# Performance work log

Measured on AMD Instinct MI355X. Metric: run time of the kernel, lower is better.

The kernel has to match this reference:

```python
import jax, jax.numpy as jnp
import numpy as np

HM = 256  # output_hm_shape


def _peak_grid(heatmap):
    # max_num_peaks=1 NMS -> global argmax per (b, joint) channel
    B, J, H, W = heatmap.shape
    idx = jnp.argmax(heatmap.reshape(B, J, H * W), axis=-1)
    y = (idx // W).astype(jnp.float32)
    x = (idx % W).astype(jnp.float32)
    ny = (H - 1) / 2.0
    nx = (W - 1) / 2.0
    # normalized (gx, gy) in [-1, 1], note (row,col) -> (x,y) flip as in source
    return jnp.stack([(x - nx) / nx, (y - ny) / ny], axis=-1)  # [B, J, 2]


def _bilinear_sample(feat, grid):
    # feat: [B, C, H, W], grid: [B, N, 2] (gx, gy), align_corners=True
    B, C, H, W = feat.shape
    x = (grid[..., 0] + 1.0) * 0.5 * (W - 1)
    y = (grid[..., 1] + 1.0) * 0.5 * (H - 1)
    x0 = jnp.floor(x); y0 = jnp.floor(y)
    wx = x - x0; wy = y - y0
    x0i = jnp.clip(x0, 0, W - 1).astype(jnp.int32)
    x1i = jnp.clip(x0 + 1, 0, W - 1).astype(jnp.int32)
    y0i = jnp.clip(y0, 0, H - 1).astype(jnp.int32)
    y1i = jnp.clip(y0 + 1, 0, H - 1).astype(jnp.int32)
    ff = feat.reshape(B, C, H * W)
    def g(iy, ix):
        return jnp.take_along_axis(ff, (iy * W + ix)[:, None, :], axis=2)  # [B, C, N]
    wx = wx[:, None, :]; wy = wy[:, None, :]
    return (g(y0i, x0i) * (1 - wx) * (1 - wy) + g(y0i, x1i) * wx * (1 - wy)
            + g(y1i, x0i) * (1 - wx) * wy + g(y1i, x1i) * wx * wy)


def _nearest_sample(feat, grid):
    B, C, H, W = feat.shape
    ix = jnp.clip(jnp.round((grid[..., 0] + 1.0) * 0.5 * (W - 1)), 0, W - 1).astype(jnp.int32)
    iy = jnp.clip(jnp.round((grid[..., 1] + 1.0) * 0.5 * (H - 1)), 0, H - 1).astype(jnp.int32)
    ff = feat.reshape(B, C, H * W)
    return jnp.take_along_axis(ff, (iy * W + ix)[:, None, :], axis=2)  # [B, C, N]


def _mlp(x, Ws, bs):
    # ReLU on every layer including last (is_activation_last=True)
    for W, b in zip(Ws, bs):
        x = jax.nn.relu(x @ W + b)
    return x


def setup_inputs() -> dict:
    key = jax.random.key(0)
    ks = jax.random.split(key, 16)
    inp = {
        'heatmap': jax.random.normal(ks[0], (16, 64, HM, HM), jnp.float32),
        'pos_embed': jax.random.normal(ks[1], (16, 32, HM, HM), jnp.float32),
        'feat1': jax.random.normal(ks[2], (16, 96, 128, 128), jnp.float32),
        'feat2': jax.random.normal(ks[3], (16, 384, 64, 64), jnp.float32),
        'feat3': jax.random.normal(ks[4], (16, 512, 32, 32), jnp.float32),
    }
    dims = [992, 1024, 512, 256, 224]
    for i in range(4):
        fan = dims[i]
        inp[f'W{i+1}'] = jax.random.normal(ks[5 + i], (dims[i], dims[i + 1]), jnp.float32) / np.sqrt(fan)
        inp[f'b{i+1}'] = jnp.zeros((dims[i + 1],), jnp.float32)
    return inp


def reference(heatmap, pos_embed, feat1, feat2, feat3, W1, b1, W2, b2, W3, b3, W4, b4):
    grid = _peak_grid(heatmap)  # [B, J, 2], detached in original (cpu numpy)
    positions = _nearest_sample(pos_embed, grid)  # [B, 32, J]
    ms = jnp.concatenate([_bilinear_sample(feat1, grid),
                          _bilinear_sample(feat2, grid),
                          _bilinear_sample(feat3, grid)], axis=1)  # [B, 992, J]
    seq = _mlp(ms.transpose(0, 2, 1), [W1, W2, W3, W4], [b1, b2, b3, b4])  # [B, J, 224]
    input_seq = jnp.concatenate([seq.transpose(0, 2, 1), positions], axis=1)  # [B, 256, J]
    return input_seq
```

## Files before the change

kernel.cpp:

```cpp
#include <hip/hip_runtime.h>
#include <hip/hip_bf16.h>
#include <cstddef>
#include <cstdint>


typedef __attribute__((ext_vector_type(8))) short bf16x8;
typedef __attribute__((ext_vector_type(4))) float f32x4;

__device__ inline void bilinear_block(const float* __restrict__ fb, int C, int H, int W,
                                      float gx, float gy,
                                      __hip_bfloat16* __restrict__ dst, int tid) {
    const float x = (gx + 1.0f) * 0.5f * (float)(W - 1);
    const float y = (gy + 1.0f) * 0.5f * (float)(H - 1);
    const float x0f = floorf(x), y0f = floorf(y);
    const float wx = x - x0f, wy = y - y0f;
    const int x0 = (int)fminf(fmaxf(x0f,       0.f), (float)(W - 1));
    const int x1 = (int)fminf(fmaxf(x0f + 1.f, 0.f), (float)(W - 1));
    const int y0 = (int)fminf(fmaxf(y0f,       0.f), (float)(H - 1));
    const int y1 = (int)fminf(fmaxf(y0f + 1.f, 0.f), (float)(H - 1));
    const float w00 = (1.f - wx) * (1.f - wy);
    const float w01 = wx * (1.f - wy);
    const float w10 = (1.f - wx) * wy;
    const float w11 = wx * wy;
    const int i00 = y0 * W + x0, i01 = y0 * W + x1;
    const int i10 = y1 * W + x0, i11 = y1 * W + x1;
    const size_t HW = (size_t)H * W;
    for (int c = tid; c < C; c += 256) {
        const float* fc = fb + (size_t)c * HW;
        float v = fc[i00] * w00 + fc[i01] * w01 + fc[i10] * w10 + fc[i11] * w11;
        dst[c] = __float2bfloat16(v);
    }
}

__global__ __launch_bounds__(256) void fused_front_kernel(
    const float* __restrict__ hm,
    const float* __restrict__ pos_embed,
    const float* __restrict__ feat1, const float* __restrict__ feat2,
    const float* __restrict__ feat3,
    const float* __restrict__ W1, const float* __restrict__ W2,
    const float* __restrict__ W3, const float* __restrict__ W4,
    __hip_bfloat16* __restrict__ T1, __hip_bfloat16* __restrict__ T2,
    __hip_bfloat16* __restrict__ T3, __hip_bfloat16* __restrict__ T4,
    __hip_bfloat16* __restrict__ X0, float* __restrict__ out) {
    __shared__ float smem[32 * 33];
    float* sval = smem;
    int*   sidx = (int*)(smem + 4);
    const int tid = threadIdx.x;

    if (blockIdx.x >= 1024) {
        int bid = blockIdx.x - 1024;
        const float* W; __hip_bfloat16* T; int K, N;
        if (bid < 992)        { W = W1; T = T1; K = 992;  N = 1024; }
        else if (bid < 1504)  { bid -= 992;  W = W2; T = T2; K = 1024; N = 512; }
        else if (bid < 1632)  { bid -= 1504; W = W3; T = T3; K = 512;  N = 256; }
        else                  { bid -= 1632; W = W4; T = T4; K = 256;  N = 224; }
        const int tilesN = N >> 5;
        const int tk = bid / tilesN, tn = bid - tk * tilesN;
        float (*tile)[33] = (float(*)[33])smem;
        const int col = tid & 31, rowg = tid >> 5;
        #pragma unroll
        for (int i = 0; i < 4; ++i) {
            int k = (tk << 5) + rowg + (i << 3);
            tile[rowg + (i << 3)][col] = W[(size_t)k * N + (tn << 5) + col];
        }
        __syncthreads();
        #pragma unroll
        for (int i = 0; i < 4; ++i) {
            int n = (tn << 5) + rowg + (i << 3);
            T[(size_t)n * K + (tk << 5) + col] = __float2bfloat16(tile[col][rowg + (i << 3)]);
        }
        return;
    }

    const int plane = blockIdx.x;
    const float4* p4 = (const float4*)(hm + (size_t)plane * 65536);
    float best = -3.402823466e38f;
    int bidx = 0;
    for (int i = tid; i < 16384; i += 256) {
        float4 v = p4[i];
        int base = i << 2;
        if (v.x > best) { best = v.x; bidx = base; }
        if (v.y > best) { best = v.y; bidx = base + 1; }
        if (v.z > best) { best = v.z; bidx = base + 2; }
        if (v.w > best) { best = v.w; bidx = base + 3; }
    }
    #pragma unroll
    for (int off = 32; off > 0; off >>= 1) {
        float ov = __shfl_down(best, off);
        int   oi = __shfl_down(bidx, off);
        if (ov > best || (ov == best && oi < bidx)) { best = ov; bidx = oi; }
    }
    if ((tid & 63) == 0) { sval[tid >> 6] = best; sidx[tid >> 6] = bidx; }
    __syncthreads();
    float bv = sval[0]; int bi = sidx[0];
    #pragma unroll
    for (int w2 = 1; w2 < 4; ++w2) {
        float ov = sval[w2]; int oi = sidx[w2];
        if (ov > bv || (ov == bv && oi < bi)) { bv = ov; bi = oi; }
    }
    const int idx = bi;

    const int b = plane >> 6, j = plane & 63;
    const int py = idx >> 8, px = idx & 255;
    const float gx = ((float)px - 127.5f) / 127.5f;
    const float gy = ((float)py - 127.5f) / 127.5f;

    if (tid < 32) {
        float v = pos_embed[((size_t)(b * 32 + tid)) * 65536 + idx];
        out[(size_t)b * 16384 + (size_t)(224 + tid) * 64 + j] = v;
    }

    __hip_bfloat16* xrow = X0 + (size_t)plane * 992;
    bilinear_block(feat1 + (size_t)b *  96 * 128 * 128,  96, 128, 128, gx, gy, xrow,       tid);
    bilinear_block(feat2 + (size_t)b * 384 *  64 *  64, 384,  64,  64, gx, gy, xrow +  96, tid);
    bilinear_block(feat3 + (size_t)b * 512 *  32 *  32, 512,  32,  32, gx, gy, xrow + 480, tid);
}

template<bool LAST>
__global__ __launch_bounds__(256) void mfma_gemm_sk(
    const short* __restrict__ A, const short* __restrict__ Bt,
    const float* __restrict__ bias, void* __restrict__ Yv,
    int N, int K) {
    __shared__ float red[4 * 64 * 17];
    const int tid = threadIdx.x;
    const int w = tid >> 6, lane = tid & 63;
    const int q = lane >> 4, r = lane & 15;
    const int m0 = blockIdx.y << 5;
    const int n0 = blockIdx.x << 5;

    const short* pa0 = A  + (size_t)(m0 + r) * K + (q << 3);
    const short* pa1 = pa0 + (size_t)16 * K;
    const short* pb0 = Bt + (size_t)(n0 + r) * K + (q << 3);
    const short* pb1 = pb0 + (size_t)16 * K;

    f32x4 acc00 = {0.f,0.f,0.f,0.f}, acc01 = {0.f,0.f,0.f,0.f};
    f32x4 acc10 = {0.f,0.f,0.f,0.f}, acc11 = {0.f,0.f,0.f,0.f};

    const int nk = K >> 5;
    int ks = w;
    {
        int off = ks << 5;
        bf16x8 a0 = *(const bf16x8*)(pa0 + off);
        bf16x8 a1 = *(const bf16x8*)(pa1 + off);
        bf16x8 b0 = *(const bf16x8*)(pb0 + off);
        bf16x8 b1 = *(const bf16x8*)(pb1 + off);
        for (ks += 4; ks < nk; ks += 4) {
            int o2 = ks << 5;
            bf16x8 na0 = *(const bf16x8*)(pa0 + o2);
            bf16x8 na1 = *(const bf16x8*)(pa1 + o2);
            bf16x8 nb0 = *(const bf16x8*)(pb0 + o2);
            bf16x8 nb1 = *(const bf16x8*)(pb1 + o2);
            acc00 = __builtin_amdgcn_mfma_f32_16x16x32_bf16(a0, b0, acc00, 0, 0, 0);
            acc01 = __builtin_amdgcn_mfma_f32_16x16x32_bf16(a0, b1, acc01, 0, 0, 0);
            acc10 = __builtin_amdgcn_mfma_f32_16x16x32_bf16(a1, b0, acc10, 0, 0, 0);
            acc11 = __builtin_amdgcn_mfma_f32_16x16x32_bf16(a1, b1, acc11, 0, 0, 0);
            a0 = na0; a1 = na1; b0 = nb0; b1 = nb1;
        }
        acc00 = __builtin_amdgcn_mfma_f32_16x16x32_bf16(a0, b0, acc00, 0, 0, 0);
        acc01 = __builtin_amdgcn_mfma_f32_16x16x32_bf16(a0, b1, acc01, 0, 0, 0);
        acc10 = __builtin_amdgcn_mfma_f32_16x16x32_bf16(a1, b0, acc10, 0, 0, 0);
        acc11 = __builtin_amdgcn_mfma_f32_16x16x32_bf16(a1, b1, acc11, 0, 0, 0);
    }

    float* myrow = red + (size_t)(w * 64 + lane) * 17;
    #pragma unroll
    for (int i = 0; i < 4; ++i) {
        myrow[i]      = acc00[i];
        myrow[4 + i]  = acc01[i];
        myrow[8 + i]  = acc10[i];
        myrow[12 + i] = acc11[i];
    }
    __syncthreads();

    #pragma unroll
    for (int jj = 0; jj < 4; ++jj) {
        const int e = tid + (jj << 8);
        const int le = e >> 4, s = e & 15;
        const int which = s >> 2, i = s & 3;
        float v = red[(0 * 64 + le) * 17 + s] + red[(1 * 64 + le) * 17 + s]
                + red[(2 * 64 + le) * 17 + s] + red[(3 * 64 + le) * 17 + s];
        const int qe = le >> 4, re = le & 15;
        const int row = m0 + (qe << 2) + i + ((which & 2) ? 16 : 0);
        const int col = n0 + re + ((which & 1) ? 16 : 0);
        v = fmaxf(v + bias[col], 0.f);
        if (LAST) {
            float* O = (float*)Yv;
            O[(size_t)(row >> 6) * 16384 + (size_t)col * 64 + (row & 63)] = v;
        } else {
            __hip_bfloat16* Y = (__hip_bfloat16*)Yv;
            Y[(size_t)row * N + col] = __float2bfloat16(v);
        }
    }
}

extern "C" void kernel_launch(void* const* d_in, const int* in_sizes, int n_in,
                              void* d_out, int out_size, void* d_ws, size_t ws_size,
                              hipStream_t stream) {
    (void)in_sizes; (void)n_in; (void)out_size; (void)ws_size;
    const float* heatmap   = (const float*)d_in[0];
    const float* pos_embed = (const float*)d_in[1];
    const float* feat1     = (const float*)d_in[2];
    const float* feat2     = (const float*)d_in[3];
    const float* feat3     = (const float*)d_in[4];
    const float* W1 = (const float*)d_in[5];  const float* b1 = (const float*)d_in[6];
    const float* W2 = (const float*)d_in[7];  const float* b2 = (const float*)d_in[8];
    const float* W3 = (const float*)d_in[9];  const float* b3 = (const float*)d_in[10];
    const float* W4 = (const float*)d_in[11]; const float* b4 = (const float*)d_in[12];
    float* out = (float*)d_out;

    char* ws = (char*)d_ws;
    short* X0 = (short*)(ws + 8192);
    short* X1 = X0 + (size_t)1024 * 992;
    short* X2 = X1 + (size_t)1024 * 1024;
    short* X3 = X2 + (size_t)1024 * 512;
    short* T1 = X3 + (size_t)1024 * 256;
    short* T2 = T1 + (size_t)1024 * 992;
    short* T3 = T2 + (size_t)512 * 1024;
    short* T4 = T3 + (size_t)256 * 512;

    fused_front_kernel<<<2712, 256, 0, stream>>>(
        heatmap, pos_embed, feat1, feat2, feat3,
        W1, W2, W3, W4,
        (__hip_bfloat16*)T1, (__hip_bfloat16*)T2, (__hip_bfloat16*)T3, (__hip_bfloat16*)T4,
        (__hip_bfloat16*)X0, out);
    mfma_gemm_sk<false><<<dim3(32, 32), 256, 0, stream>>>(X0, T1, b1, X1, 1024,  992);
    mfma_gemm_sk<false><<<dim3(16, 32), 256, 0, stream>>>(X1, T2, b2, X2,  512, 1024);
    mfma_gemm_sk<false><<<dim3( 8, 32), 256, 0, stream>>>(X2, T3, b3, X3,  256,  512);
    mfma_gemm_sk<true ><<<dim3( 7, 32), 256, 0, stream>>>(X3, T4, b4, out,  224,  256);
}
```

Measured before the change: 578.1 us.

## Merge front and four GEMM launches into one cooperative persistent kernel

Replaces the front kernel and the four GEMM kernel launches with a single cooperative kernel of 512 blocks. The blocks loop over argmax planes, weight transposes and GEMM tiles, with grid.sync between layers. GEMM tiles are resized per layer so each stage has about 1024 tiles. This removes launch gaps and tail effects between kernels, but it halves the parallelism of the bandwidth-bound heatmap argmax phase and adds grid-wide barrier cost.

```diff
diff --git a/kernel.cpp b/kernel.cpp
--- a/kernel.cpp
+++ b/kernel.cpp
@@ -1,15 +1,18 @@
 #include <hip/hip_runtime.h>
+#include <hip/hip_cooperative_groups.h>
 #include <hip/hip_bf16.h>
 #include <cstddef>
 #include <cstdint>
 
+namespace cg = cooperative_groups;
+
 
 typedef __attribute__((ext_vector_type(8))) short bf16x8;
 typedef __attribute__((ext_vector_type(4))) float f32x4;
 
-__device__ inline void bilinear_block(const float* __restrict__ fb, int C, int H, int W,
-                                      float gx, float gy,
-                                      __hip_bfloat16* __restrict__ dst, int tid) {
+__device__ __forceinline__ void bilinear_block(const float* __restrict__ fb, int C, int H, int W,
+                                               float gx, float gy,
+                                               __hip_bfloat16* __restrict__ dst, int tid) {
     const float x = (gx + 1.0f) * 0.5f * (float)(W - 1);
     const float y = (gy + 1.0f) * 0.5f * (float)(H - 1);
     const float x0f = floorf(x), y0f = floorf(y);
@@ -32,156 +35,87 @@
     }
 }
 
-__global__ __launch_bounds__(256) void fused_front_kernel(
-    const float* __restrict__ hm,
-    const float* __restrict__ pos_embed,
-    const float* __restrict__ feat1, const float* __restrict__ feat2,
-    const float* __restrict__ feat3,
-    const float* __restrict__ W1, const float* __restrict__ W2,
-    const float* __restrict__ W3, const float* __restrict__ W4,
-    __hip_bfloat16* __restrict__ T1, __hip_bfloat16* __restrict__ T2,
-    __hip_bfloat16* __restrict__ T3, __hip_bfloat16* __restrict__ T4,
-    __hip_bfloat16* __restrict__ X0, float* __restrict__ out) {
-    __shared__ float smem[32 * 33];
-    float* sval = smem;
-    int*   sidx = (int*)(smem + 4);
-    const int tid = threadIdx.x;
-
-    if (blockIdx.x >= 1024) {
-        int bid = blockIdx.x - 1024;
-        const float* W; __hip_bfloat16* T; int K, N;
-        if (bid < 992)        { W = W1; T = T1; K = 992;  N = 1024; }
-        else if (bid < 1504)  { bid -= 992;  W = W2; T = T2; K = 1024; N = 512; }
-        else if (bid < 1632)  { bid -= 1504; W = W3; T = T3; K = 512;  N = 256; }
-        else                  { bid -= 1632; W = W4; T = T4; K = 256;  N = 224; }
-        const int tilesN = N >> 5;
-        const int tk = bid / tilesN, tn = bid - tk * tilesN;
-        float (*tile)[33] = (float(*)[33])smem;
-        const int col = tid & 31, rowg = tid >> 5;
-        #pragma unroll
-        for (int i = 0; i < 4; ++i) {
-            int k = (tk << 5) + rowg + (i << 3);
-            tile[rowg + (i << 3)][col] = W[(size_t)k * N + (tn << 5) + col];
-        }
-        __syncthreads();
-        #pragma unroll
-        for (int i = 0; i < 4; ++i) {
-            int n = (tn << 5) + rowg + (i << 3);
-            T[(size_t)n * K + (tk << 5) + col] = __float2bfloat16(tile[col][rowg + (i << 3)]);
-        }
-        return;
-    }
-
-    const int plane = blockIdx.x;
-    const float4* p4 = (const float4*)(hm + (size_t)plane * 65536);
-    float best = -3.402823466e38f;
-    int bidx = 0;
-    for (int i = tid; i < 16384; i += 256) {
-        float4 v = p4[i];
-        int base = i << 2;
-        if (v.x > best) { best = v.x; bidx = base; }
-        if (v.y > best) { best = v.y; bidx = base + 1; }
-        if (v.z > best) { best = v.z; bidx = base + 2; }
-        if (v.w > best) { best = v.w; bidx = base + 3; }
-    }
-    #pragma unroll
-    for (int off = 32; off > 0; off >>= 1) {
-        float ov = __shfl_down(best, off);
-        int   oi = __shfl_down(bidx, off);
-        if (ov > best || (ov == best && oi < bidx)) { best = ov; bidx = oi; }
-    }
-    if ((tid & 63) == 0) { sval[tid >> 6] = best; sidx[tid >> 6] = bidx; }
-    __syncthreads();
-    float bv = sval[0]; int bi = sidx[0];
-    #pragma unroll
-    for (int w2 = 1; w2 < 4; ++w2) {
-        float ov = sval[w2]; int oi = sidx[w2];
-        if (ov > bv || (ov == bv && oi < bi)) { bv = ov; bi = oi; }
-    }
-    const int idx = bi;
-
-    const int b = plane >> 6, j = plane & 63;
-    const int py = idx >> 8, px = idx & 255;
-    const float gx = ((float)px - 127.5f) / 127.5f;
-    const float gy = ((float)py - 127.5f) / 127.5f;
-
-    if (tid < 32) {
-        float v = pos_embed[((size_t)(b * 32 + tid)) * 65536 + idx];
-        out[(size_t)b * 16384 + (size_t)(224 + tid) * 64 + j] = v;
-    }
-
-    __hip_bfloat16* xrow = X0 + (size_t)plane * 992;
-    bilinear_block(feat1 + (size_t)b *  96 * 128 * 128,  96, 128, 128, gx, gy, xrow,       tid);
-    bilinear_block(feat2 + (size_t)b * 384 *  64 *  64, 384,  64,  64, gx, gy, xrow +  96, tid);
-    bilinear_block(feat3 + (size_t)b * 512 *  32 *  32, 512,  32,  32, gx, gy, xrow + 480, tid);
-}
-
-template<bool LAST>
-__global__ __launch_bounds__(256) void mfma_gemm_sk(
+template<int AR, int BR, bool LAST>
+__device__ __forceinline__ void gemm_tile(
     const short* __restrict__ A, const short* __restrict__ Bt,
     const float* __restrict__ bias, void* __restrict__ Yv,
-    int N, int K) {
-    __shared__ float red[4 * 64 * 17];
-    const int tid = threadIdx.x;
+    const int N, const int K, const int m0, const int n0,
+    float* __restrict__ red, const int tid) {
     const int w = tid >> 6, lane = tid & 63;
     const int q = lane >> 4, r = lane & 15;
-    const int m0 = blockIdx.y << 5;
-    const int n0 = blockIdx.x << 5;
-
-    const short* pa0 = A  + (size_t)(m0 + r) * K + (q << 3);
-    const short* pa1 = pa0 + (size_t)16 * K;
-    const short* pb0 = Bt + (size_t)(n0 + r) * K + (q << 3);
-    const short* pb1 = pb0 + (size_t)16 * K;
-
-    f32x4 acc00 = {0.f,0.f,0.f,0.f}, acc01 = {0.f,0.f,0.f,0.f};
-    f32x4 acc10 = {0.f,0.f,0.f,0.f}, acc11 = {0.f,0.f,0.f,0.f};
+
+    const short* pa[AR];
+    const short* pb[BR];
+    pa[0] = A + (size_t)(m0 + r) * K + (q << 3);
+    #pragma unroll
+    for (int i = 1; i < AR; ++i) pa[i] = pa[i - 1] + (size_t)16 * K;
+    pb[0] = Bt + (size_t)(n0 + r) * K + (q << 3);
+    #pragma unroll
+    for (int j = 1; j < BR; ++j) pb[j] = pb[j - 1] + (size_t)16 * K;
+
+    f32x4 acc[AR][BR];
+    #pragma unroll
+    for (int i = 0; i < AR; ++i)
+        #pragma unroll
+        for (int j = 0; j < BR; ++j)
+            acc[i][j] = (f32x4){0.f, 0.f, 0.f, 0.f};
 
     const int nk = K >> 5;
-    int ks = w;
+    bf16x8 a[AR], b[BR];
     {
-        int off = ks << 5;
-        bf16x8 a0 = *(const bf16x8*)(pa0 + off);
-        bf16x8 a1 = *(const bf16x8*)(pa1 + off);
-        bf16x8 b0 = *(const bf16x8*)(pb0 + off);
-        bf16x8 b1 = *(const bf16x8*)(pb1 + off);
-        for (ks += 4; ks < nk; ks += 4) {
-            int o2 = ks << 5;
-            bf16x8 na0 = *(const bf16x8*)(pa0 + o2);
-            bf16x8 na1 = *(const bf16x8*)(pa1 + o2);
-            bf16x8 nb0 = *(const bf16x8*)(pb0 + o2);
-            bf16x8 nb1 = *(const bf16x8*)(pb1 + o2);
-            acc00 = __builtin_amdgcn_mfma_f32_16x16x32_bf16(a0, b0, acc00, 0, 0, 0);
-            acc01 = __builtin_amdgcn_mfma_f32_16x16x32_bf16(a0, b1, acc01, 0, 0, 0);
-            acc10 = __builtin_amdgcn_mfma_f32_16x16x32_bf16(a1, b0, acc10, 0, 0, 0);
-            acc11 = __builtin_amdgcn_mfma_f32_16x16x32_bf16(a1, b1, acc11, 0, 0, 0);
-            a0 = na0; a1 = na1; b0 = nb0; b1 = nb1;
-        }
-        acc00 = __builtin_amdgcn_mfma_f32_16x16x32_bf16(a0, b0, acc00, 0, 0, 0);
-        acc01 = __builtin_amdgcn_mfma_f32_16x16x32_bf16(a0, b1, acc01, 0, 0, 0);
-        acc10 = __builtin_amdgcn_mfma_f32_16x16x32_bf16(a1, b0, acc10, 0, 0, 0);
-        acc11 = __builtin_amdgcn_mfma_f32_16x16x32_bf16(a1, b1, acc11, 0, 0, 0);
-    }
-
-    float* myrow = red + (size_t)(w * 64 + lane) * 17;
-    #pragma unroll
-    for (int i = 0; i < 4; ++i) {
-        myrow[i]      = acc00[i];
-        myrow[4 + i]  = acc01[i];
-        myrow[8 + i]  = acc10[i];
-        myrow[12 + i] = acc11[i];
-    }
+        const int off = w << 5;
+        #pragma unroll
+        for (int i = 0; i < AR; ++i) a[i] = *(const bf16x8*)(pa[i] + off);
+        #pragma unroll
+        for (int j = 0; j < BR; ++j) b[j] = *(const bf16x8*)(pb[j] + off);
+    }
+    for (int ks = w + 4; ks < nk; ks += 4) {
+        const int off = ks << 5;
+        bf16x8 na[AR], nb[BR];
+        #pragma unroll
+        for (int i = 0; i < AR; ++i) na[i] = *(const bf16x8*)(pa[i] + off);
+        #pragma unroll
+        for (int j = 0; j < BR; ++j) nb[j] = *(const bf16x8*)(pb[j] + off);
+        #pragma unroll
+        for (int i = 0; i < AR; ++i)
+            #pragma unroll
+            for (int j = 0; j < BR; ++j)
+                acc[i][j] = __builtin_amdgcn_mfma_f32_16x16x32_bf16(a[i], b[j], acc[i][j], 0, 0, 0);
+        #pragma unroll
+        for (int i = 0; i < AR; ++i) a[i] = na[i];
+        #pragma unroll
+        for (int j = 0; j < BR; ++j) b[j] = nb[j];
+    }
+    #pragma unroll
+    for (int i = 0; i < AR; ++i)
+        #pragma unroll
+        for (int j = 0; j < BR; ++j)
+            acc[i][j] = __builtin_amdgcn_mfma_f32_16x16x32_bf16(a[i], b[j], acc[i][j], 0, 0, 0);
+
+    constexpr int RL = AR * BR * 4;
+    constexpr int STRIDE = RL + 1;
+    float* myrow = red + (size_t)(w * 64 + lane) * STRIDE;
+    #pragma unroll
+    for (int i = 0; i < AR; ++i)
+        #pragma unroll
+        for (int j = 0; j < BR; ++j)
+            #pragma unroll
+            for (int t = 0; t < 4; ++t)
+                myrow[(i * BR + j) * 4 + t] = acc[i][j][t];
     __syncthreads();
 
     #pragma unroll
-    for (int jj = 0; jj < 4; ++jj) {
+    for (int jj = 0; jj < AR * BR; ++jj) {
         const int e = tid + (jj << 8);
-        const int le = e >> 4, s = e & 15;
-        const int which = s >> 2, i = s & 3;
-        float v = red[(0 * 64 + le) * 17 + s] + red[(1 * 64 + le) * 17 + s]
-                + red[(2 * 64 + le) * 17 + s] + red[(3 * 64 + le) * 17 + s];
+        const int le = e / RL;
+        const int s  = e - le * RL;
+        const int frag = s >> 2, i = s & 3;
+        const int ar = frag / BR, br = frag - (frag / BR) * BR;
+        float v = red[(0 * 64 + le) * STRIDE + s] + red[(1 * 64 + le) * STRIDE + s]
+                + red[(2 * 64 + le) * STRIDE + s] + red[(3 * 64 + le) * STRIDE + s];
         const int qe = le >> 4, re = le & 15;
-        const int row = m0 + (qe << 2) + i + ((which & 2) ? 16 : 0);
-        const int col = n0 + re + ((which & 1) ? 16 : 0);
+        const int row = m0 + ar * 16 + (qe << 2) + i;
+        const int col = n0 + br * 16 + re;
         v = fmaxf(v + bias[col], 0.f);
         if (LAST) {
             float* O = (float*)Yv;
@@ -191,6 +125,109 @@
             Y[(size_t)row * N + col] = __float2bfloat16(v);
         }
     }
+    __syncthreads();
+}
+
+__global__ __launch_bounds__(256, 4) void mega_kernel(
+    const float* __restrict__ hm, const float* __restrict__ pos_embed,
+    const float* __restrict__ feat1, const float* __restrict__ feat2,
+    const float* __restrict__ feat3,
+    const float* __restrict__ W1, const float* __restrict__ W2,
+    const float* __restrict__ W3, const float* __restrict__ W4,
+    const float* __restrict__ b1, const float* __restrict__ b2,
+    const float* __restrict__ b3, const float* __restrict__ b4,
+    short* __restrict__ T1, short* __restrict__ T2,
+    short* __restrict__ T3, short* __restrict__ T4,
+    short* __restrict__ X0, short* __restrict__ X1,
+    short* __restrict__ X2, short* __restrict__ X3,
+    float* __restrict__ out) {
+    __shared__ float smem[4 * 64 * 17];
+    const int tid = threadIdx.x;
+    const int bid = blockIdx.x;
+    cg::grid_group grid = cg::this_grid();
+
+    for (int plane = bid; plane < 1024; plane += 512) {
+        const float4* p4 = (const float4*)(hm + (size_t)plane * 65536);
+        float best = -3.402823466e38f;
+        int bidx = 0;
+        for (int i2 = tid; i2 < 16384; i2 += 256) {
+            float4 v = p4[i2];
+            int base = i2 << 2;
+            if (v.x > best) { best = v.x; bidx = base; }
+            if (v.y > best) { best = v.y; bidx = base + 1; }
+            if (v.z > best) { best = v.z; bidx = base + 2; }
+            if (v.w > best) { best = v.w; bidx = base + 3; }
+        }
+        #pragma unroll
+        for (int off = 32; off > 0; off >>= 1) {
+            float ov = __shfl_down(best, off);
+            int   oi = __shfl_down(bidx, off);
+            if (ov > best || (ov == best && oi < bidx)) { best = ov; bidx = oi; }
+        }
+        float* sval = smem;
+        int*   sidx = (int*)(smem + 4);
+        if ((tid & 63) == 0) { sval[tid >> 6] = best; sidx[tid >> 6] = bidx; }
+        __syncthreads();
+        float bv = sval[0]; int bi = sidx[0];
+        #pragma unroll
+        for (int w2 = 1; w2 < 4; ++w2) {
+            float ov = sval[w2]; int oi = sidx[w2];
+            if (ov > bv || (ov == bv && oi < bi)) { bv = ov; bi = oi; }
+        }
+        const int idx = bi;
+        __syncthreads();
+
+        const int b = plane >> 6, j = plane & 63;
+        const int py = idx >> 8, px = idx & 255;
+        const float gx = ((float)px - 127.5f) / 127.5f;
+        const float gy = ((float)py - 127.5f) / 127.5f;
+        if (tid < 32) {
+            float v = pos_embed[((size_t)(b * 32 + tid)) * 65536 + idx];
+            out[(size_t)b * 16384 + (size_t)(224 + tid) * 64 + j] = v;
+        }
+        __hip_bfloat16* xrow = (__hip_bfloat16*)X0 + (size_t)plane * 992;
+        bilinear_block(feat1 + (size_t)b *  96 * 128 * 128,  96, 128, 128, gx, gy, xrow,       tid);
+        bilinear_block(feat2 + (size_t)b * 384 *  64 *  64, 384,  64,  64, gx, gy, xrow +  96, tid);
+        bilinear_block(feat3 + (size_t)b * 512 *  32 *  32, 512,  32,  32, gx, gy, xrow + 480, tid);
+    }
+
+    for (int t = bid; t < 1688; t += 512) {
+        int bb = t;
+        const float* W; __hip_bfloat16* T; int K, N;
+        if (bb < 992)        { W = W1; T = (__hip_bfloat16*)T1; K = 992;  N = 1024; }
+        else if (bb < 1504)  { bb -= 992;  W = W2; T = (__hip_bfloat16*)T2; K = 1024; N = 512; }
+        else if (bb < 1632)  { bb -= 1504; W = W3; T = (__hip_bfloat16*)T3; K = 512;  N = 256; }
+        else                 { bb -= 1632; W = W4; T = (__hip_bfloat16*)T4; K = 256;  N = 224; }
+        const int tilesN = N >> 5;
+        const int tk = bb / tilesN, tn = bb - tk * tilesN;
+        float (*tile)[33] = (float(*)[33])smem;
+        const int col = tid & 31, rowg = tid >> 5;
+        #pragma unroll
+        for (int i = 0; i < 4; ++i) {
+            int k = (tk << 5) + rowg + (i << 3);
+            tile[rowg + (i << 3)][col] = W[(size_t)k * N + (tn << 5) + col];
+        }
+        __syncthreads();
+        #pragma unroll
+        for (int i = 0; i < 4; ++i) {
+            int n = (tn << 5) + rowg + (i << 3);
+            T[(size_t)n * K + (tk << 5) + col] = __float2bfloat16(tile[col][rowg + (i << 3)]);
+        }
+        __syncthreads();
+    }
+
+    grid.sync();
+    for (int t = bid; t < 1024; t += 512)
+        gemm_tile<2, 2, false>(X0, T1, b1, X1, 1024,  992, (t >> 5) << 5, (t & 31) << 5, smem, tid);
+    grid.sync();
+    for (int t = bid; t < 1024; t += 512)
+        gemm_tile<1, 2, false>(X1, T2, b2, X2,  512, 1024, (t >> 4) << 4, (t & 15) << 5, smem, tid);
+    grid.sync();
+    for (int t = bid; t < 1024; t += 512)
+        gemm_tile<1, 1, false>(X2, T3, b3, X3,  256,  512, (t >> 4) << 4, (t & 15) << 4, smem, tid);
+    grid.sync();
+    for (int t = bid; t < 896; t += 512)
+        gemm_tile<1, 1, true>(X3, T4, b4, out, 224,  256, (t / 14) << 4, (t % 14) << 4, smem, tid);
 }
 
 extern "C" void kernel_launch(void* const* d_in, const int* in_sizes, int n_in,
@@ -218,13 +255,14 @@
     short* T3 = T2 + (size_t)512 * 1024;
     short* T4 = T3 + (size_t)256 * 512;
 
-    fused_front_kernel<<<2712, 256, 0, stream>>>(
-        heatmap, pos_embed, feat1, feat2, feat3,
-        W1, W2, W3, W4,
-        (__hip_bfloat16*)T1, (__hip_bfloat16*)T2, (__hip_bfloat16*)T3, (__hip_bfloat16*)T4,
-        (__hip_bfloat16*)X0, out);
-    mfma_gemm_sk<false><<<dim3(32, 32), 256, 0, stream>>>(X0, T1, b1, X1, 1024,  992);
-    mfma_gemm_sk<false><<<dim3(16, 32), 256, 0, stream>>>(X1, T2, b2, X2,  512, 1024);
-    mfma_gemm_sk<false><<<dim3( 8, 32), 256, 0, stream>>>(X2, T3, b3, X3,  256,  512);
-    mfma_gemm_sk<true ><<<dim3( 7, 32), 256, 0, stream>>>(X3, T4, b4, out,  224,  256);
-}
+    void* args[] = {
+        (void*)&heatmap, (void*)&pos_embed,
+        (void*)&feat1, (void*)&feat2, (void*)&feat3,
+        (void*)&W1, (void*)&W2, (void*)&W3, (void*)&W4,
+        (void*)&b1, (void*)&b2, (void*)&b3, (void*)&b4,
+        (void*)&T1, (void*)&T2, (void*)&T3, (void*)&T4,
+        (void*)&X0, (void*)&X1, (void*)&X2, (void*)&X3,
+        (void*)&out };
+    hipLaunchCooperativeKernel(reinterpret_cast<void*>(mega_kernel),
+                               dim3(512), dim3(256), args, 0, stream);
+}
```

After: 844.1 us. 1.46x slower.
